# Performance work log

Hardware: AMD Instinct MI355X
Metric: run time of the kernel (lower is better)

The kernel has to match this reference:

```python
import jax, jax.numpy as jnp
import numpy as np

B, C, H, W = 4, 256, 64, 64
CQ = C // 8


def setup_inputs() -> dict:
    key = jax.random.key(0)
    ks = jax.random.split(key, 7)
    x = jax.random.normal(ks[0], (B, C, H, W), dtype=jnp.float32)
    Wq = jax.random.normal(ks[1], (CQ, C), dtype=jnp.float32) * 0.02
    bq = jnp.zeros((CQ,), dtype=jnp.float32)
    Wk = jax.random.normal(ks[2], (CQ, C), dtype=jnp.float32) * 0.02
    bk = jnp.zeros((CQ,), dtype=jnp.float32)
    Wv = jax.random.normal(ks[3], (C, C), dtype=jnp.float32) * 0.02
    bv = jnp.zeros((C,), dtype=jnp.float32)
    return {"x": x, "Wq": Wq, "bq": bq, "Wk": Wk, "bk": bk, "Wv": Wv, "bv": bv}


def reference(x, Wq, bq, Wk, bk, Wv, bv):
    b, c, h, w = x.shape
    n = h * w
    xf = x.reshape(b, c, n)                                   # [B,C,N]
    # 1x1 convs are per-pixel GEMMs
    q = jnp.einsum('qc,bcn->bnq', Wq, xf) + bq                # [B,N,Cq]
    k = jnp.einsum('qc,bcn->bqn', Wk, xf) + bk[None, :, None] # [B,Cq,N]
    v = jnp.einsum('vc,bcn->bnv', Wv, xf) + bv                # [B,N,C]
    scale = float(n) ** 0.5
    energy = jnp.einsum('bnq,bqm->bnm', q, k) / scale         # [B,N,N]
    attn = jax.nn.softmax(energy, axis=-1)
    out = jnp.einsum('bnm,bmv->bnv', attn, v)                 # [B,N,C]
    # Faithful to torch's out.view(B,C,H,W) applied to the contiguous [B,N,C]
    # tensor: a raw memory reinterpretation, NOT a transpose.
    return out.reshape(b, c, h, w)
```

## Files before the change

kernel.cpp:

```cpp
#include <hip/hip_runtime.h>

#define BATCH 4
#define CH    256
#define NPIX  4096
#define CQD   32

typedef __bf16 bf16;
typedef bf16 bf16x8 __attribute__((ext_vector_type(8)));
typedef bf16 bf16x4 __attribute__((ext_vector_type(4)));
typedef float f32x4 __attribute__((ext_vector_type(4)));
typedef float f32x16 __attribute__((ext_vector_type(16)));

#define MFMA16 __builtin_amdgcn_mfma_f32_16x16x32_bf16
#define MFMA32 __builtin_amdgcn_mfma_f32_32x32x16_bf16

#define GLOAD_LDS16(g, l) __builtin_amdgcn_global_load_lds( \
    (const __attribute__((address_space(1))) void*)(g),     \
    (__attribute__((address_space(3))) void*)(l), 16, 0, 0)

__global__ __launch_bounds__(256) void prep_kernel(
    const float* __restrict__ Wq, const float* __restrict__ bq,
    const float* __restrict__ Wk, const float* __restrict__ bk,
    const float* __restrict__ Wv, const float* __restrict__ bv,
    bf16* __restrict__ Wb, float* __restrict__ bb)
{
    int r = blockIdx.x, c = threadIdx.x;
    const float* W; const float* bs; float sc; int rr;
    if (r < 32)      { W = Wq; bs = bq; sc = 0.015625f; rr = r; }
    else if (r < 64) { W = Wk; bs = bk; sc = 1.0f;      rr = r - 32; }
    else             { W = Wv; bs = bv; sc = 1.0f;      rr = r - 64; }
    Wb[(size_t)r * CH + c] = (bf16)(W[(size_t)rr * CH + c] * sc);
    if (c == 0) bb[r] = bs[rr] * sc;
}

__global__ __launch_bounds__(256) void proj_kernel(
    const float* __restrict__ x,
    const bf16* __restrict__ Wb, const float* __restrict__ bb,
    bf16* __restrict__ qp, bf16* __restrict__ kp, bf16* __restrict__ vT)
{
    __shared__ __align__(16) bf16 xT[32][264];
    __shared__ __align__(16) bf16 vstage[4][16][40];

    const int t  = threadIdx.x;
    const int b  = blockIdx.x >> 7;
    const int n0 = (blockIdx.x & 127) << 5;
    const int w    = t >> 6;
    const int lane = t & 63;
    const int l16  = t & 15;
    const int quad = (t & 63) >> 4;

    const float* xb = x + (size_t)b * CH * NPIX;
#pragma unroll
    for (int j = 0; j < 8; ++j) {
        int id = t + j * 256;
        int c  = id >> 3;
        int n4 = (id & 7) << 2;
        float4 vv = *(const float4*)(xb + (size_t)c * NPIX + n0 + n4);
        xT[n4 + 0][c] = (bf16)vv.x;
        xT[n4 + 1][c] = (bf16)vv.y;
        xT[n4 + 2][c] = (bf16)vv.z;
        xT[n4 + 3][c] = (bf16)vv.w;
    }
    __syncthreads();

    for (int rt = 0; rt < 5; ++rt) {
        int ro = w * 80 + rt * 16;
        int kind = (ro < 32) ? 0 : (ro < 64) ? 1 : 2;

        bf16x8 afrag[8];
        const bf16* wrow = Wb + (size_t)(ro + l16) * CH + quad * 8;
#pragma unroll
        for (int kc = 0; kc < 8; ++kc)
            afrag[kc] = *(const bf16x8*)(wrow + kc * 32);
        float bv4[4];
#pragma unroll
        for (int r = 0; r < 4; ++r) bv4[r] = bb[ro + quad * 4 + r];

#pragma unroll
        for (int nt = 0; nt < 2; ++nt) {
            f32x4 acc = {0.f, 0.f, 0.f, 0.f};
#pragma unroll
            for (int kc = 0; kc < 8; ++kc) {
                bf16x8 bfr = *(const bf16x8*)&xT[nt * 16 + l16][kc * 32 + quad * 8];
                acc = MFMA16(afrag[kc], bfr, acc, 0, 0, 0);
            }
            if (kind != 2) {
                bf16x4 pk;
#pragma unroll
                for (int r = 0; r < 4; ++r)
                    pk[r] = (bf16)(acc[r] + bv4[r]);
                int n = n0 + nt * 16 + l16;
                int col = (kind == 0 ? ro : ro - 32) + quad * 4;
                bf16* dst = (kind == 0) ? qp : kp;
                *(bf16x4*)&dst[((size_t)b * NPIX + n) * CQD + col] = pk;
            } else {
#pragma unroll
                for (int r = 0; r < 4; ++r)
                    vstage[w][quad * 4 + r][nt * 16 + l16] = (bf16)(acc[r] + bv4[r]);
            }
        }
        if (kind == 2) {
            int vrow = lane >> 2, vcc = lane & 3;
            bf16x8 chunk = *(const bf16x8*)&vstage[w][vrow][vcc * 8];
            *(bf16x8*)&vT[((size_t)b * CH + (ro - 64) + vrow) * NPIX + n0 + vcc * 8] = chunk;
        }
    }
}

template<int S, bool DIRECT>
__global__ __launch_bounds__(256, 2) void attn_kernel(
    const bf16* __restrict__ qp, const bf16* __restrict__ kp,
    const bf16* __restrict__ vT,
    bf16* __restrict__ Opart, float* __restrict__ Lpart,
    float* __restrict__ out)
{
    __shared__ __align__(16) bf16 Vt[2][256][64];
    __shared__ __align__(16) bf16 PbS[128][64];

    const int t    = threadIdx.x;
    const int bid  = blockIdx.x;
    const int s    = bid % S;
    const int tq   = bid / S;
    const int b    = tq >> 5;
    const int qt   = tq & 31;
    const int n0   = qt << 7;
    const int w    = t >> 6;
    const int lane = t & 63;
    const int l16  = t & 15;
    const int quad = (t & 63) >> 4;
    const int sw   = l16 & 7;
    const int l32  = lane & 31;
    const int h    = lane >> 5;
    const int qh   = w >> 1;
    const int chb  = (w & 1) * 128;

    const bf16* qpb = qp + ((size_t)b * NPIX + n0 + w * 32) * CQD;
    bf16x8 qfrag[2];
    qfrag[0] = *(const bf16x8*)(qpb + (size_t)l16 * CQD + quad * 8);
    qfrag[1] = *(const bf16x8*)(qpb + (size_t)(16 + l16) * CQD + quad * 8);

    f32x16 o[2][4];
#pragma unroll
    for (int i = 0; i < 2; ++i)
#pragma unroll
        for (int j = 0; j < 4; ++j)
#pragma unroll
            for (int r = 0; r < 16; ++r) o[i][j][r] = 0.f;
    float lsum[2] = {0.f, 0.f};

    const bf16* kpb = kp + (size_t)b * NPIX * CQD;
    const bf16* vTb = vT + (size_t)b * CH * NPIX;
    const int k0 = s * (NPIX / S);
    const int iters = NPIX / S / 64;

    const int vrow_off = lane >> 3;
    const int vchunk   = (lane & 7) ^ vrow_off;
    auto issue_vt = [&](int buf, int m0) {
#pragma unroll
        for (int j = 0; j < 8; ++j) {
            int rowbase = j * 32 + w * 8;
            const bf16* src = vTb + (size_t)(rowbase + vrow_off) * NPIX + m0 + vchunk * 8;
            GLOAD_LDS16(src, &Vt[buf][rowbase][0]);
        }
    };
    auto load_kf = [&](int m0, bf16x8* kf) {
#pragma unroll
        for (int mt = 0; mt < 4; ++mt)
            kf[mt] = *(const bf16x8*)(kpb + (size_t)(m0 + mt * 16 + l16) * CQD + quad * 8);
    };

    bf16x8 kfa[4], kfb[4];
    issue_vt(0, k0);
    load_kf(k0, kfa);
    __syncthreads();

    for (int mi = 0; mi < iters; ++mi) {
        const int cur = mi & 1;
        const int m0  = k0 + (mi << 6);
        if (mi + 1 < iters) {
            issue_vt(cur ^ 1, m0 + 64);
            load_kf(m0 + 64, kfb);
        }

        f32x4 sv[2][4];
#pragma unroll
        for (int mt = 0; mt < 4; ++mt) {
            f32x4 z = {0.f, 0.f, 0.f, 0.f};
            sv[0][mt] = MFMA16(kfa[mt], qfrag[0], z, 0, 0, 0);
            sv[1][mt] = MFMA16(kfa[mt], qfrag[1], z, 0, 0, 0);
        }

#pragma unroll
        for (int g = 0; g < 2; ++g) {
            float rs = 0.f;
#pragma unroll
            for (int mt = 0; mt < 4; ++mt) {
                bf16x4 pk;
#pragma unroll
                for (int r = 0; r < 4; ++r) {
                    float e = __expf(sv[g][mt][r]);
                    rs += e;
                    pk[r] = (bf16)e;
                }
                int slot = (2 * mt + (quad >> 1)) ^ sw;
                *(bf16x4*)&PbS[w * 32 + g * 16 + l16][slot * 8 + (quad & 1) * 4] = pk;
            }
            lsum[g] += rs;
        }
        __syncthreads();

        bf16x8 pA[2][4];
#pragma unroll
        for (int t32 = 0; t32 < 2; ++t32)
#pragma unroll
            for (int kg = 0; kg < 4; ++kg) {
                int row = qh * 64 + t32 * 32 + l32;
                pA[t32][kg] = *(const bf16x8*)&PbS[row][((2 * kg + h) ^ (l32 & 7)) * 8];
            }
#pragma unroll
        for (int ct = 0; ct < 4; ++ct) {
            int vrow = chb + ct * 32 + l32;
            bf16x8 vB[4];
#pragma unroll
            for (int kg = 0; kg < 4; ++kg)
                vB[kg] = *(const bf16x8*)&Vt[cur][vrow][((2 * kg + h) ^ (l32 & 7)) * 8];
#pragma unroll
            for (int t32 = 0; t32 < 2; ++t32)
#pragma unroll
                for (int kg = 0; kg < 4; ++kg)
                    o[t32][ct] = MFMA32(pA[t32][kg], vB[kg], o[t32][ct], 0, 0, 0);
        }
        __syncthreads();
#pragma unroll
        for (int i = 0; i < 4; ++i) kfa[i] = kfb[i];
    }

    float l_g[2];
#pragma unroll
    for (int g = 0; g < 2; ++g) {
        float v = lsum[g];
        v += __shfl_xor(v, 16);
        v += __shfl_xor(v, 32);
        l_g[g] = v;
    }
    float* lsh = (float*)PbS;
    if (quad == 0) {
#pragma unroll
        for (int g = 0; g < 2; ++g)
            lsh[w * 32 + g * 16 + l16] = l_g[g];
    }
    __syncthreads();

    const size_t prb2 = ((size_t)s * BATCH + b) * NPIX + n0;
    if (!DIRECT && quad == 0) {
#pragma unroll
        for (int g = 0; g < 2; ++g)
            Lpart[prb2 + w * 32 + g * 16 + l16] = l_g[g];
    }

    bf16* eb = (bf16*)Vt + (size_t)w * 32 * 136;
#pragma unroll
    for (int t32 = 0; t32 < 2; ++t32) {
        float rinv[16];
#pragma unroll
        for (int reg = 0; reg < 16; ++reg) {
            int q_r = (reg & 3) + 8 * (reg >> 2) + 4 * h;
            rinv[reg] = 1.0f / lsh[qh * 64 + t32 * 32 + q_r];
        }
        if (!DIRECT) {
#pragma unroll
            for (int ct = 0; ct < 4; ++ct)
#pragma unroll
                for (int reg = 0; reg < 16; ++reg) {
                    int q_r = (reg & 3) + 8 * (reg >> 2) + 4 * h;
                    eb[q_r * 136 + ct * 32 + l32] = (bf16)(o[t32][ct][reg] * rinv[reg]);
                }
            int vrow = lane >> 4, vcc = lane & 15;
#pragma unroll
            for (int p = 0; p < 8; ++p) {
                int row = p * 4 + vrow;
                bf16x8 chunk = *(const bf16x8*)&eb[row * 136 + vcc * 8];
                *(bf16x8*)&Opart[(prb2 + qh * 64 + t32 * 32 + row) * CH +
                                 chb + vcc * 8] = chunk;
            }
        } else {
            float* ob = out + (prb2 + qh * 64 + t32 * 32) * CH + chb;
#pragma unroll
            for (int ct = 0; ct < 4; ++ct)
#pragma unroll
                for (int reg = 0; reg < 16; ++reg) {
                    int q_r = (reg & 3) + 8 * (reg >> 2) + 4 * h;
                    ob[(size_t)q_r * CH + ct * 32 + l32] = o[t32][ct][reg] * rinv[reg];
                }
        }
    }
}

template<int S>
__global__ __launch_bounds__(256) void combine_kernel(
    const bf16* __restrict__ Opart, const float* __restrict__ Lpart,
    float* __restrict__ out)
{
    int idx  = blockIdx.x * 256 + threadIdx.x;
    int nrow = idx >> 5;
    int cc   = (idx & 31) * 8;
    int b    = nrow >> 12, nin = nrow & 4095;

    size_t pr[S];
    float  ls[S], wsum = 0.f;
#pragma unroll
    for (int s = 0; s < S; ++s) {
        pr[s] = ((size_t)s * BATCH + b) * NPIX + nin;
        ls[s] = Lpart[pr[s]];
        wsum += ls[s];
    }
    float inv = 1.0f / wsum;

    float acc[8] = {0.f, 0.f, 0.f, 0.f, 0.f, 0.f, 0.f, 0.f};
#pragma unroll
    for (int s = 0; s < S; ++s) {
        bf16x8 ov = *(const bf16x8*)&Opart[pr[s] * CH + cc];
        float wn = ls[s] * inv;
#pragma unroll
        for (int j = 0; j < 8; ++j) acc[j] += wn * (float)ov[j];
    }
    float4 o0 = {acc[0], acc[1], acc[2], acc[3]};
    float4 o1 = {acc[4], acc[5], acc[6], acc[7]};
    *(float4*)&out[(size_t)nrow * CH + cc]     = o0;
    *(float4*)&out[(size_t)nrow * CH + cc + 4] = o1;
}

extern "C" void kernel_launch(void* const* d_in, const int* in_sizes, int n_in,
                              void* d_out, int out_size, void* d_ws, size_t ws_size,
                              hipStream_t stream) {
    const float* x  = (const float*)d_in[0];
    const float* Wq = (const float*)d_in[1];
    const float* bq = (const float*)d_in[2];
    const float* Wk = (const float*)d_in[3];
    const float* bk = (const float*)d_in[4];
    const float* Wv = (const float*)d_in[5];
    const float* bv = (const float*)d_in[6];
    float* out = (float*)d_out;

    char* ws = (char*)d_ws;
    const size_t qpB   = (size_t)BATCH * NPIX * CQD * 2;
    const size_t vTB   = (size_t)BATCH * CH * NPIX * 2;
    const size_t WbB   = (size_t)320 * CH * 2;
    const size_t bbB   = 320 * 4 + 768;
    const size_t baseB = 2 * qpB + vTB + WbB + bbB;
    const size_t oprtB = (size_t)BATCH * NPIX * CH * 2;
    const size_t mlB   = (size_t)BATCH * NPIX * 4;

    bf16*  qp = (bf16*)ws;
    bf16*  kp = (bf16*)(ws + qpB);
    bf16*  vT = (bf16*)(ws + 2 * qpB);
    bf16*  Wb = (bf16*)(ws + 2 * qpB + vTB);
    float* bb = (float*)(ws + 2 * qpB + vTB + WbB);

    prep_kernel<<<dim3(320), dim3(256), 0, stream>>>(Wq, bq, Wk, bk, Wv, bv, Wb, bb);
    proj_kernel<<<dim3(BATCH * (NPIX / 32)), dim3(256), 0, stream>>>(
        x, Wb, bb, qp, kp, vT);

    auto need = [&](int S) { return baseB + (size_t)S * (oprtB + mlB); };
    int S = (ws_size >= need(4)) ? 4 : (ws_size >= need(2)) ? 2
          : (ws_size >= need(1)) ? 1 : 0;

    if (S > 0) {
        bf16*  Opart = (bf16*)(ws + baseB);
        float* Lpart = (float*)(ws + baseB + (size_t)S * oprtB);
        if (S == 4) {
            attn_kernel<4, false><<<dim3(128 * 4), dim3(256), 0, stream>>>(
                qp, kp, vT, Opart, Lpart, out);
            combine_kernel<4><<<dim3(2048), dim3(256), 0, stream>>>(Opart, Lpart, out);
        } else if (S == 2) {
            attn_kernel<2, false><<<dim3(128 * 2), dim3(256), 0, stream>>>(
                qp, kp, vT, Opart, Lpart, out);
            combine_kernel<2><<<dim3(2048), dim3(256), 0, stream>>>(Opart, Lpart, out);
        } else {
            attn_kernel<1, false><<<dim3(128), dim3(256), 0, stream>>>(
                qp, kp, vT, Opart, Lpart, out);
            combine_kernel<1><<<dim3(2048), dim3(256), 0, stream>>>(Opart, Lpart, out);
        }
    } else {
        attn_kernel<1, true><<<dim3(128), dim3(256), 0, stream>>>(
            qp, kp, vT, nullptr, nullptr, out);
    }
}
```

Measured before the change: 141.9 us.

## Split attention work across eight waves per block and use exp2 softmax

The attention block grows from 4 to 8 waves (512 threads). Each wave now owns 16 query rows for the QK step and a 64-channel quarter of V for the PV step, which halves per-wave accumulator registers and aims for more latency hiding. The log2(e) factor is folded into the Wq scaling so exp2f can replace __expf. K fragments are loaded directly each iteration instead of double-buffered in registers, and s_setprio is raised around the MFMA section. The risks are exposed K load latency and more waves contending for the block barriers.

```diff
diff --git a/kernel.cpp b/kernel.cpp
--- a/kernel.cpp
+++ b/kernel.cpp
@@ -26,7 +26,7 @@
 {
     int r = blockIdx.x, c = threadIdx.x;
     const float* W; const float* bs; float sc; int rr;
-    if (r < 32)      { W = Wq; bs = bq; sc = 0.015625f; rr = r; }
+    if (r < 32)      { W = Wq; bs = bq; sc = 0.015625f * 1.44269504088896340736f; rr = r; }
     else if (r < 64) { W = Wk; bs = bk; sc = 1.0f;      rr = r - 32; }
     else             { W = Wv; bs = bv; sc = 1.0f;      rr = r - 64; }
     Wb[(size_t)r * CH + c] = (bf16)(W[(size_t)rr * CH + c] * sc);
@@ -108,7 +108,7 @@
 }
 
 template<int S, bool DIRECT>
-__global__ __launch_bounds__(256, 2) void attn_kernel(
+__global__ __launch_bounds__(512, 4) void attn_kernel(
     const bf16* __restrict__ qp, const bf16* __restrict__ kp,
     const bf16* __restrict__ vT,
     bf16* __restrict__ Opart, float* __restrict__ Lpart,
@@ -131,22 +131,20 @@
     const int sw   = l16 & 7;
     const int l32  = lane & 31;
     const int h    = lane >> 5;
-    const int qh   = w >> 1;
-    const int chb  = (w & 1) * 128;
-
-    const bf16* qpb = qp + ((size_t)b * NPIX + n0 + w * 32) * CQD;
-    bf16x8 qfrag[2];
-    qfrag[0] = *(const bf16x8*)(qpb + (size_t)l16 * CQD + quad * 8);
-    qfrag[1] = *(const bf16x8*)(qpb + (size_t)(16 + l16) * CQD + quad * 8);
-
-    f32x16 o[2][4];
+    const int qh   = w >> 2;
+    const int chq  = (w & 3) * 64;
+
+    const bf16* qpb = qp + ((size_t)b * NPIX + n0 + w * 16) * CQD;
+    bf16x8 qfrag = *(const bf16x8*)(qpb + (size_t)l16 * CQD + quad * 8);
+
+    f32x16 o[2][2];
 #pragma unroll
     for (int i = 0; i < 2; ++i)
 #pragma unroll
-        for (int j = 0; j < 4; ++j)
+        for (int j = 0; j < 2; ++j)
 #pragma unroll
             for (int r = 0; r < 16; ++r) o[i][j][r] = 0.f;
-    float lsum[2] = {0.f, 0.f};
+    float lsum = 0.f;
 
     const bf16* kpb = kp + (size_t)b * NPIX * CQD;
     const bf16* vTb = vT + (size_t)b * CH * NPIX;
@@ -157,108 +155,85 @@
     const int vchunk   = (lane & 7) ^ vrow_off;
     auto issue_vt = [&](int buf, int m0) {
 #pragma unroll
-        for (int j = 0; j < 8; ++j) {
-            int rowbase = j * 32 + w * 8;
+        for (int j = 0; j < 4; ++j) {
+            int rowbase = j * 64 + w * 8;
             const bf16* src = vTb + (size_t)(rowbase + vrow_off) * NPIX + m0 + vchunk * 8;
             GLOAD_LDS16(src, &Vt[buf][rowbase][0]);
         }
     };
-    auto load_kf = [&](int m0, bf16x8* kf) {
-#pragma unroll
-        for (int mt = 0; mt < 4; ++mt)
-            kf[mt] = *(const bf16x8*)(kpb + (size_t)(m0 + mt * 16 + l16) * CQD + quad * 8);
-    };
-
-    bf16x8 kfa[4], kfb[4];
+
     issue_vt(0, k0);
-    load_kf(k0, kfa);
     __syncthreads();
 
     for (int mi = 0; mi < iters; ++mi) {
         const int cur = mi & 1;
         const int m0  = k0 + (mi << 6);
-        if (mi + 1 < iters) {
-            issue_vt(cur ^ 1, m0 + 64);
-            load_kf(m0 + 64, kfb);
-        }
-
-        f32x4 sv[2][4];
+        if (mi + 1 < iters) issue_vt(cur ^ 1, m0 + 64);
+
+        bf16x8 kf[4];
+#pragma unroll
+        for (int mt = 0; mt < 4; ++mt)
+            kf[mt] = *(const bf16x8*)(kpb + (size_t)(m0 + mt * 16 + l16) * CQD + quad * 8);
+
+        f32x4 sv[4];
 #pragma unroll
         for (int mt = 0; mt < 4; ++mt) {
             f32x4 z = {0.f, 0.f, 0.f, 0.f};
-            sv[0][mt] = MFMA16(kfa[mt], qfrag[0], z, 0, 0, 0);
-            sv[1][mt] = MFMA16(kfa[mt], qfrag[1], z, 0, 0, 0);
-        }
-
-#pragma unroll
-        for (int g = 0; g < 2; ++g) {
-            float rs = 0.f;
-#pragma unroll
-            for (int mt = 0; mt < 4; ++mt) {
-                bf16x4 pk;
-#pragma unroll
-                for (int r = 0; r < 4; ++r) {
-                    float e = __expf(sv[g][mt][r]);
-                    rs += e;
-                    pk[r] = (bf16)e;
-                }
-                int slot = (2 * mt + (quad >> 1)) ^ sw;
-                *(bf16x4*)&PbS[w * 32 + g * 16 + l16][slot * 8 + (quad & 1) * 4] = pk;
+            sv[mt] = MFMA16(kf[mt], qfrag, z, 0, 0, 0);
+        }
+
+#pragma unroll
+        for (int mt = 0; mt < 4; ++mt) {
+            bf16x4 pk;
+#pragma unroll
+            for (int r = 0; r < 4; ++r) {
+                float e = exp2f(sv[mt][r]);
+                lsum += e;
+                pk[r] = (bf16)e;
             }
-            lsum[g] += rs;
+            int slot = (2 * mt + (quad >> 1)) ^ sw;
+            *(bf16x4*)&PbS[w * 16 + l16][slot * 8 + (quad & 1) * 4] = pk;
         }
         __syncthreads();
 
-        bf16x8 pA[2][4];
-#pragma unroll
-        for (int t32 = 0; t32 < 2; ++t32)
-#pragma unroll
-            for (int kg = 0; kg < 4; ++kg) {
-                int row = qh * 64 + t32 * 32 + l32;
-                pA[t32][kg] = *(const bf16x8*)&PbS[row][((2 * kg + h) ^ (l32 & 7)) * 8];
-            }
-#pragma unroll
-        for (int ct = 0; ct < 4; ++ct) {
-            int vrow = chb + ct * 32 + l32;
-            bf16x8 vB[4];
+        bf16x8 vB[2][4];
+#pragma unroll
+        for (int ct = 0; ct < 2; ++ct) {
+            int vrow = chq + ct * 32 + l32;
 #pragma unroll
             for (int kg = 0; kg < 4; ++kg)
-                vB[kg] = *(const bf16x8*)&Vt[cur][vrow][((2 * kg + h) ^ (l32 & 7)) * 8];
-#pragma unroll
-            for (int t32 = 0; t32 < 2; ++t32)
+                vB[ct][kg] = *(const bf16x8*)&Vt[cur][vrow][((2 * kg + h) ^ (l32 & 7)) * 8];
+        }
+        __builtin_amdgcn_s_setprio(1);
+#pragma unroll
+        for (int t32 = 0; t32 < 2; ++t32) {
+            bf16x8 pA[4];
+            int prow = qh * 64 + t32 * 32 + l32;
+#pragma unroll
+            for (int kg = 0; kg < 4; ++kg)
+                pA[kg] = *(const bf16x8*)&PbS[prow][((2 * kg + h) ^ (l32 & 7)) * 8];
+#pragma unroll
+            for (int ct = 0; ct < 2; ++ct)
 #pragma unroll
                 for (int kg = 0; kg < 4; ++kg)
-                    o[t32][ct] = MFMA32(pA[t32][kg], vB[kg], o[t32][ct], 0, 0, 0);
-        }
+                    o[t32][ct] = MFMA32(pA[kg], vB[ct][kg], o[t32][ct], 0, 0, 0);
+        }
+        __builtin_amdgcn_s_setprio(0);
         __syncthreads();
-#pragma unroll
-        for (int i = 0; i < 4; ++i) kfa[i] = kfb[i];
-    }
-
-    float l_g[2];
-#pragma unroll
-    for (int g = 0; g < 2; ++g) {
-        float v = lsum[g];
-        v += __shfl_xor(v, 16);
-        v += __shfl_xor(v, 32);
-        l_g[g] = v;
-    }
+    }
+
+    float lv = lsum;
+    lv += __shfl_xor(lv, 16);
+    lv += __shfl_xor(lv, 32);
     float* lsh = (float*)PbS;
-    if (quad == 0) {
-#pragma unroll
-        for (int g = 0; g < 2; ++g)
-            lsh[w * 32 + g * 16 + l16] = l_g[g];
-    }
+    if (quad == 0) lsh[w * 16 + l16] = lv;
     __syncthreads();
 
     const size_t prb2 = ((size_t)s * BATCH + b) * NPIX + n0;
-    if (!DIRECT && quad == 0) {
-#pragma unroll
-        for (int g = 0; g < 2; ++g)
-            Lpart[prb2 + w * 32 + g * 16 + l16] = l_g[g];
-    }
-
-    bf16* eb = (bf16*)Vt + (size_t)w * 32 * 136;
+    if (!DIRECT && quad == 0)
+        Lpart[prb2 + w * 16 + l16] = lv;
+
+    bf16* eb = (bf16*)Vt + (size_t)w * 2176;
 #pragma unroll
     for (int t32 = 0; t32 < 2; ++t32) {
         float rinv[16];
@@ -269,24 +244,24 @@
         }
         if (!DIRECT) {
 #pragma unroll
-            for (int ct = 0; ct < 4; ++ct)
+            for (int ct = 0; ct < 2; ++ct)
 #pragma unroll
                 for (int reg = 0; reg < 16; ++reg) {
                     int q_r = (reg & 3) + 8 * (reg >> 2) + 4 * h;
-                    eb[q_r * 136 + ct * 32 + l32] = (bf16)(o[t32][ct][reg] * rinv[reg]);
+                    eb[q_r * 68 + ct * 32 + l32] = (bf16)(o[t32][ct][reg] * rinv[reg]);
                 }
-            int vrow = lane >> 4, vcc = lane & 15;
-#pragma unroll
-            for (int p = 0; p < 8; ++p) {
-                int row = p * 4 + vrow;
-                bf16x8 chunk = *(const bf16x8*)&eb[row * 136 + vcc * 8];
+            int vrow = lane >> 3, vcc = lane & 7;
+#pragma unroll
+            for (int p = 0; p < 4; ++p) {
+                int row = p * 8 + vrow;
+                bf16x8 chunk = *(const bf16x8*)&eb[row * 68 + vcc * 8];
                 *(bf16x8*)&Opart[(prb2 + qh * 64 + t32 * 32 + row) * CH +
-                                 chb + vcc * 8] = chunk;
+                                 chq + vcc * 8] = chunk;
             }
         } else {
-            float* ob = out + (prb2 + qh * 64 + t32 * 32) * CH + chb;
-#pragma unroll
-            for (int ct = 0; ct < 4; ++ct)
+            float* ob = out + (prb2 + qh * 64 + t32 * 32) * CH + chq;
+#pragma unroll
+            for (int ct = 0; ct < 2; ++ct)
 #pragma unroll
                 for (int reg = 0; reg < 16; ++reg) {
                     int q_r = (reg & 3) + 8 * (reg >> 2) + 4 * h;
@@ -369,20 +344,20 @@
         bf16*  Opart = (bf16*)(ws + baseB);
         float* Lpart = (float*)(ws + baseB + (size_t)S * oprtB);
         if (S == 4) {
-            attn_kernel<4, false><<<dim3(128 * 4), dim3(256), 0, stream>>>(
+            attn_kernel<4, false><<<dim3(128 * 4), dim3(512), 0, stream>>>(
                 qp, kp, vT, Opart, Lpart, out);
             combine_kernel<4><<<dim3(2048), dim3(256), 0, stream>>>(Opart, Lpart, out);
         } else if (S == 2) {
-            attn_kernel<2, false><<<dim3(128 * 2), dim3(256), 0, stream>>>(
+            attn_kernel<2, false><<<dim3(128 * 2), dim3(512), 0, stream>>>(
                 qp, kp, vT, Opart, Lpart, out);
             combine_kernel<2><<<dim3(2048), dim3(256), 0, stream>>>(Opart, Lpart, out);
         } else {
-            attn_kernel<1, false><<<dim3(128), dim3(256), 0, stream>>>(
+            attn_kernel<1, false><<<dim3(128), dim3(512), 0, stream>>>(
                 qp, kp, vT, Opart, Lpart, out);
             combine_kernel<1><<<dim3(2048), dim3(256), 0, stream>>>(Opart, Lpart, out);
         }
     } else {
-        attn_kernel<1, true><<<dim3(128), dim3(256), 0, stream>>>(
+        attn_kernel<1, true><<<dim3(128), dim3(512), 0, stream>>>(
             qp, kp, vT, nullptr, nullptr, out);
     }
 }
```

Result: slower. 178.8 us (+26.0%).
